# Kernel optimization log

Measured on AMD Instinct MI355X. Metric: run time of the kernel, lower is better.

Reference implementation:

```python
import jax, jax.numpy as jnp
import numpy as np

D_MODEL = 2048
NUM_HEADS = 16
HEAD_DIM = D_MODEL // NUM_HEADS
BATCH = 2
SEQ = 2048


def setup_inputs() -> dict:
    key = jax.random.key(0)
    ks = jax.random.split(key, 5)
    s = 1.0 / np.sqrt(D_MODEL)
    return {
        "x": jax.random.normal(ks[0], (BATCH, SEQ, D_MODEL), dtype=jnp.float32),
        "Wq": jax.random.normal(ks[1], (D_MODEL, D_MODEL), dtype=jnp.float32) * s,
        "Wk": jax.random.normal(ks[2], (D_MODEL, D_MODEL), dtype=jnp.float32) * s,
        "Wv": jax.random.normal(ks[3], (D_MODEL, D_MODEL), dtype=jnp.float32) * s,
        "Wo": jax.random.normal(ks[4], (D_MODEL, D_MODEL), dtype=jnp.float32) * s,
    }


def reference(x, Wq, Wk, Wv, Wo):
    B, S, D = x.shape
    H, Dh = NUM_HEADS, HEAD_DIM
    # nn.Linear(bias=False): y = x @ W.T ; split_heads is a plain view (no transpose!)
    Q = (x @ Wq.T).reshape(B, H, S, Dh)
    K = (x @ Wk.T).reshape(B, H, S, Dh)
    V = (x @ Wv.T).reshape(B, H, S, Dh)
    # scores scaled by head_dim (NOT sqrt) — faithful to source
    scores = jnp.einsum("bhqd,bhkd->bhqk", Q, K) / jnp.float32(Dh)
    causal_mask = jnp.triu(jnp.ones((S, S), dtype=bool), k=1)  # True above diagonal
    scores = jnp.where(causal_mask, -jnp.inf, scores)
    attn = jax.nn.softmax(scores, axis=-1)
    out = jnp.einsum("bhqk,bhkd->bhqd", attn, V)  # [B,H,S,Dh]
    out = out.transpose(0, 2, 1, 3).reshape(B, S, D)  # merge DOES transpose
    return out @ Wo.T
```

## Files before the change

kernel.cpp:

```cpp
#include <hip/hip_runtime.h>
#include <hip/hip_bf16.h>

using bf16 = __hip_bfloat16;
typedef __attribute__((ext_vector_type(8))) short bf16x8;
typedef __attribute__((ext_vector_type(4))) float f32x4;

#define DEVI __device__ __forceinline__

constexpr int Bn = 2, Sn = 2048, Dn = 2048, Hn = 16, DHn = 128;
constexpr int Mn = Bn * Sn;

DEVI void gload_lds16(const bf16* g, bf16* l) {
  __builtin_amdgcn_global_load_lds(
      (__attribute__((address_space(1))) void*)g,
      (__attribute__((address_space(3))) void*)l,
      16, 0, 0);
}

__global__ __launch_bounds__(256) void cvt_all_k(const float* __restrict__ x,
                                                 const float* __restrict__ wq,
                                                 const float* __restrict__ wk,
                                                 const float* __restrict__ wv,
                                                 const float* __restrict__ wo,
                                                 bf16* __restrict__ xb,
                                                 bf16* __restrict__ wb) {
  const int which = blockIdx.y;
  const float* src;
  bf16* dst;
  int n8;
  if (which == 0) { src = x;  dst = xb; n8 = Mn * Dn / 8; }
  else {
    src = (which == 1) ? wq : (which == 2) ? wk : (which == 3) ? wv : wo;
    dst = wb + (size_t)(which - 1) * Dn * Dn;
    n8 = Dn * Dn / 8;
  }
  for (int i = blockIdx.x * 256 + threadIdx.x; i < n8; i += gridDim.x * 256) {
    const float4* p = (const float4*)src + (size_t)i * 2;
    float4 a = p[0], b = p[1];
    union { bf16 h[8]; bf16x8 v; } u;
    u.h[0] = __float2bfloat16(a.x); u.h[1] = __float2bfloat16(a.y);
    u.h[2] = __float2bfloat16(a.z); u.h[3] = __float2bfloat16(a.w);
    u.h[4] = __float2bfloat16(b.x); u.h[5] = __float2bfloat16(b.y);
    u.h[6] = __float2bfloat16(b.z); u.h[7] = __float2bfloat16(b.w);
    *((bf16x8*)dst + i) = u.v;
  }
}

template <int OUTF32, int NCT, int NMAT>
__global__ __launch_bounds__(512, 1) void gemm8f(const bf16* __restrict__ A,
                                                 const bf16* __restrict__ W,
                                                 void* __restrict__ Cv) {
  constexpr int K = 2048, NT = K / 64;
  constexpr int SLOTE = (128 + 256) * 64;
  __shared__ bf16 smem[3 * SLOTE];

  constexpr int MT = Mn / 128;
  const int nwg = MT * NCT;
  const int orig = blockIdx.x;
  const int wgid = (orig & 7) * (nwg >> 3) + (orig >> 3);
  const int bm = wgid / NCT;
  const int bcn = wgid % NCT;
  constexpr int nper = NCT / NMAT;
  const int z = bcn / nper;
  const int col0 = (bcn % nper) * 256;

  const int t = threadIdx.x;
  const int wave = t >> 6, lane = t & 63;
  const int wm = wave >> 2, wn = wave & 3;
  const int lr = lane & 15, lg = lane >> 4;
  const int swz = lr & 7;

  const int srow = t >> 3;
  const int schk = (t & 7) ^ (srow & 7);
  const bf16* Ab = A + (size_t)(bm * 128 + srow) * K + schk * 8;
  const bf16* Bb = W + (size_t)z * (2048 * 2048) +
                   (size_t)(col0 + srow) * K + schk * 8;

  auto stgA = [&](int slot, int kt, int u) {
    gload_lds16(Ab + (size_t)u * 64 * K + kt * 64,
                smem + slot * SLOTE + u * 4096 + t * 8);
  };
  auto stgB = [&](int slot, int kt, int u) {
    gload_lds16(Bb + (size_t)u * 64 * K + kt * 64,
                smem + slot * SLOTE + 8192 + u * 4096 + t * 8);
  };

  f32x4 acc[4][4];
  const f32x4 zf = {0.f, 0.f, 0.f, 0.f};
#pragma unroll
  for (int i = 0; i < 4; ++i)
#pragma unroll
    for (int j = 0; j < 4; ++j) acc[i][j] = zf;

  stgA(0, 0, 0); stgA(0, 0, 1);
  stgB(0, 0, 0); stgB(0, 0, 1); stgB(0, 0, 2); stgB(0, 0, 3);
  stgA(1, 1, 0); stgA(1, 1, 1);
  stgB(1, 1, 0); stgB(1, 1, 1); stgB(1, 1, 2); stgB(1, 1, 3);

  int sl = 0;
#pragma unroll 1
  for (int kt = 0; kt < NT; ++kt) {
    const bf16* sA = smem + sl * SLOTE;
    const bf16* sB = sA + 8192;
    int sl2 = sl + 2; if (sl2 >= 3) sl2 -= 3;
    const bool pf = (kt + 2 < NT);

    if (kt == NT - 1) asm volatile("s_waitcnt vmcnt(0)" ::: "memory");
    else              asm volatile("s_waitcnt vmcnt(6)" ::: "memory");
    __builtin_amdgcn_s_barrier();

    {
      bf16x8 af[4], bv[4];
#pragma unroll
      for (int i = 0; i < 4; ++i)
        af[i] = *(const bf16x8*)(sA + (wm * 64 + i * 16 + lr) * 64 + ((lg ^ swz) * 8));
#pragma unroll
      for (int n = 0; n < 4; ++n)
        bv[n] = *(const bf16x8*)(sB + (wn * 64 + n * 16 + lr) * 64 + ((lg ^ swz) * 8));
      if (pf) { stgA(sl2, kt + 2, 0); stgA(sl2, kt + 2, 1); stgB(sl2, kt + 2, 0); }
      __builtin_amdgcn_s_barrier();
      asm volatile("s_waitcnt lgkmcnt(0)" ::: "memory");
      __builtin_amdgcn_sched_barrier(0);
      __builtin_amdgcn_s_setprio(1);
#pragma unroll
      for (int i = 0; i < 4; ++i)
#pragma unroll
        for (int n = 0; n < 4; ++n)
          acc[i][n] = __builtin_amdgcn_mfma_f32_16x16x32_bf16(af[i], bv[n], acc[i][n], 0, 0, 0);
      __builtin_amdgcn_s_setprio(0);
      __builtin_amdgcn_s_barrier();
    }

    {
      bf16x8 af[4], bv[4];
#pragma unroll
      for (int i = 0; i < 4; ++i)
        af[i] = *(const bf16x8*)(sA + (wm * 64 + i * 16 + lr) * 64 + (((4 + lg) ^ swz) * 8));
#pragma unroll
      for (int n = 0; n < 4; ++n)
        bv[n] = *(const bf16x8*)(sB + (wn * 64 + n * 16 + lr) * 64 + (((4 + lg) ^ swz) * 8));
      if (pf) { stgB(sl2, kt + 2, 1); stgB(sl2, kt + 2, 2); stgB(sl2, kt + 2, 3); }
      __builtin_amdgcn_s_barrier();
      asm volatile("s_waitcnt lgkmcnt(0)" ::: "memory");
      __builtin_amdgcn_sched_barrier(0);
      __builtin_amdgcn_s_setprio(1);
#pragma unroll
      for (int i = 0; i < 4; ++i)
#pragma unroll
        for (int n = 0; n < 4; ++n)
          acc[i][n] = __builtin_amdgcn_mfma_f32_16x16x32_bf16(af[i], bv[n], acc[i][n], 0, 0, 0);
      __builtin_amdgcn_s_setprio(0);
    }

    sl = (sl == 2) ? 0 : sl + 1;
  }

  const int r0 = bm * 128 + wm * 64, c0 = col0 + wn * 64;
#pragma unroll
  for (int mm = 0; mm < 4; ++mm)
#pragma unroll
    for (int nn = 0; nn < 4; ++nn) {
      const int rr = r0 + mm * 16 + lg * 4;
      const int cc = c0 + nn * 16 + lr;
#pragma unroll
      for (int r = 0; r < 4; ++r) {
        float v = acc[mm][nn][r];
        if (OUTF32) {
          ((float*)Cv)[(size_t)(rr + r) * 2048 + cc] = v;
        } else {
          bf16* C = (bf16*)Cv + (size_t)z * (Mn * 2048);
          C[(size_t)(rr + r) * 2048 + cc] = __float2bfloat16(v);
        }
      }
    }
}

__global__ __launch_bounds__(256, 2) void transpose_v(const bf16* __restrict__ V,
                                                      bf16* __restrict__ VT) {
  __shared__ bf16 tile[128 * 128];
  const int kt = blockIdx.x, bh = blockIdx.y;
  const bf16* Vh = V + (size_t)bh * (Sn * DHn);
  bf16* VTh = VT + (size_t)bh * (DHn * Sn);
  const int t = threadIdx.x;
  const int rr = t >> 4, cc = t & 15;
#pragma unroll
  for (int i = 0; i < 8; ++i) {
    int r = rr + i * 16;
    int ch = cc ^ ((r >> 3) & 7);
    *(bf16x8*)(tile + r * 128 + ch * 8) =
        *(const bf16x8*)(Vh + (size_t)(kt * 128 + r) * DHn + cc * 8);
  }
  __syncthreads();
  const int dr = t >> 4, li = t & 15;
#pragma unroll
  for (int i = 0; i < 8; ++i) {
    int dh = dr + i * 16;
    union { bf16 h[8]; bf16x8 v; } u;
#pragma unroll
    for (int j = 0; j < 8; ++j) {
      int k = li * 8 + j;
      int ch = (dh >> 3) ^ ((k >> 3) & 7);
      u.h[j] = tile[k * 128 + ch * 8 + (dh & 7)];
    }
    *(bf16x8*)(VTh + (size_t)dh * Sn + kt * 128 + li * 8) = u.v;
  }
}

__global__ __launch_bounds__(512, 1) void attn_k3(const bf16* __restrict__ Q,
                                                  const bf16* __restrict__ K,
                                                  const bf16* __restrict__ VT,
                                                  bf16* __restrict__ Mg) {
  __shared__ bf16 smem[40960];
  bf16* sK0 = smem;
  bf16* sK1 = smem + 8192;
  bf16* sV0 = smem + 16384;
  bf16* sV1 = smem + 24576;
  bf16* sP  = smem + 32768;
  bf16* sO  = smem;

  const int bi = blockIdx.x;
  const int xcd = bi & 7, slt = bi >> 3;
  const int bh = (slt & 3) * 8 + xcd;
  const int j = slt >> 2;
  const bf16* Qh = Q + (size_t)bh * (Sn * DHn);
  const bf16* Kh = K + (size_t)bh * (Sn * DHn);
  const bf16* VTh = VT + (size_t)bh * (DHn * Sn);
  const int b = bh >> 4, h = bh & 15;

  const int t = threadIdx.x, wave = t >> 6, lane = t & 63;
  const int lr = lane & 15, lg = lane >> 4;

  auto STAGE = [&](int buf, int kt) {
    bf16* dK = buf ? sK1 : sK0;
    bf16* dV = buf ? sV1 : sV0;
#pragma unroll
    for (int i = 0; i < 2; ++i) {
      int c = i * 512 + t;
      int row = c >> 4, c16 = c & 15;
      gload_lds16(Kh + (size_t)(kt * 64 + row) * DHn + ((c16 ^ (row & 7)) * 8),
                  dK + c * 8);
    }
#pragma unroll
    for (int i = 0; i < 2; ++i) {
      int c = i * 512 + t;
      int row = c >> 3, c8 = c & 7;
      gload_lds16(VTh + (size_t)row * Sn + kt * 64 + ((c8 ^ (row & 7)) * 8),
                  dV + c * 8);
    }
  };

  const f32x4 zf = {0.f, 0.f, 0.f, 0.f};

  for (int pi = 0; pi < 2; ++pi) {
    const int qb = pi ? (15 - j) : j;
    const int nt = qb * 2 + 2;
    const int q0 = qb * 128 + wave * 16;

    bf16x8 qf[4];
#pragma unroll
    for (int kk = 0; kk < 4; ++kk)
      qf[kk] = *(const bf16x8*)(Qh + (size_t)(q0 + lr) * DHn + kk * 32 + lg * 8);

    f32x4 o[8];
#pragma unroll
    for (int d = 0; d < 8; ++d) o[d] = zf;
    float mrun[4], lrun[4];
#pragma unroll
    for (int r = 0; r < 4; ++r) { mrun[r] = -3e38f; lrun[r] = 0.f; }

    STAGE(0, 0);
    __syncthreads();
    int cur = 0;

    for (int kt = 0; kt < nt; ++kt) {
      if (kt + 1 < nt) STAGE(cur ^ 1, kt + 1);

      bf16* sKc = cur ? sK1 : sK0;
      bf16* sVc = cur ? sV1 : sV0;

      f32x4 sfr[4];
#pragma unroll
      for (int nn = 0; nn < 4; ++nn) sfr[nn] = zf;
#pragma unroll
      for (int kk = 0; kk < 4; ++kk)
#pragma unroll
        for (int nn = 0; nn < 4; ++nn) {
          int row = nn * 16 + lr;
          int ch = (kk * 4 + lg) ^ (row & 7);
          bf16x8 kf = *(const bf16x8*)(sKc + row * DHn + ch * 8);
          sfr[nn] = __builtin_amdgcn_mfma_f32_16x16x32_bf16(qf[kk], kf, sfr[nn], 0, 0, 0);
        }

      const bool maskt = (kt >= qb * 2);
      float pv[4][4];
#pragma unroll
      for (int nn = 0; nn < 4; ++nn)
#pragma unroll
        for (int r = 0; r < 4; ++r) {
          float v = sfr[nn][r] * (1.0f / 128.0f);
          if (maskt) {
            int kg = kt * 64 + nn * 16 + lr;
            int qg = q0 + lg * 4 + r;
            if (kg > qg) v = -1e30f;
          }
          pv[nn][r] = v;
        }
      float mnew[4], alpha[4], rsum[4];
#pragma unroll
      for (int r = 0; r < 4; ++r) {
        float rm = fmaxf(fmaxf(pv[0][r], pv[1][r]), fmaxf(pv[2][r], pv[3][r]));
        rm = fmaxf(rm, __shfl_xor(rm, 1));
        rm = fmaxf(rm, __shfl_xor(rm, 2));
        rm = fmaxf(rm, __shfl_xor(rm, 4));
        rm = fmaxf(rm, __shfl_xor(rm, 8));
        mnew[r] = fmaxf(mrun[r], rm);
        alpha[r] = __expf(mrun[r] - mnew[r]);
        mrun[r] = mnew[r];
        rsum[r] = 0.f;
      }
#pragma unroll
      for (int nn = 0; nn < 4; ++nn)
#pragma unroll
        for (int r = 0; r < 4; ++r) {
          float p = __expf(pv[nn][r] - mnew[r]);
          pv[nn][r] = p;
          rsum[r] += p;
        }
#pragma unroll
      for (int r = 0; r < 4; ++r) {
        float s = rsum[r];
        s += __shfl_xor(s, 1); s += __shfl_xor(s, 2);
        s += __shfl_xor(s, 4); s += __shfl_xor(s, 8);
        lrun[r] = lrun[r] * alpha[r] + s;
      }
#pragma unroll
      for (int d = 0; d < 8; ++d)
#pragma unroll
        for (int r = 0; r < 4; ++r) o[d][r] *= alpha[r];

#pragma unroll
      for (int nn = 0; nn < 4; ++nn)
#pragma unroll
        for (int r = 0; r < 4; ++r) {
          int row = lg * 4 + r;
          int chk = (nn * 2 + (lr >> 3)) ^ (row & 7);
          sP[wave * 1024 + row * 64 + chk * 8 + (lr & 7)] = __float2bfloat16(pv[nn][r]);
        }

      bf16x8 pf[2];
#pragma unroll
      for (int kk = 0; kk < 2; ++kk) {
        int ch = (kk * 4 + lg) ^ (lr & 7);
        pf[kk] = *(const bf16x8*)(sP + wave * 1024 + lr * 64 + ch * 8);
      }
#pragma unroll
      for (int d = 0; d < 8; ++d)
#pragma unroll
        for (int kk = 0; kk < 2; ++kk) {
          int vrow = d * 16 + lr;
          int vch = (kk * 4 + lg) ^ (vrow & 7);
          bf16x8 vf = *(const bf16x8*)(sVc + vrow * 64 + vch * 8);
          o[d] = __builtin_amdgcn_mfma_f32_16x16x32_bf16(pf[kk], vf, o[d], 0, 0, 0);
        }

      __syncthreads();
      cur ^= 1;
    }

    float inv[4];
#pragma unroll
    for (int r = 0; r < 4; ++r) inv[r] = 1.0f / lrun[r];
#pragma unroll
    for (int d = 0; d < 8; ++d)
#pragma unroll
      for (int r = 0; r < 4; ++r) {
        int row = wave * 16 + lg * 4 + r;
        int col = d * 16 + lr;
        int chk = ((col >> 3) ^ (row & 7));
        sO[row * 128 + chk * 8 + (col & 7)] = __float2bfloat16(o[d][r] * inv[r]);
      }
    __syncthreads();
    bf16* Mh = Mg + ((size_t)(b * Sn + qb * 128)) * Dn + h * DHn;
#pragma unroll
    for (int i = 0; i < 4; ++i) {
      int row = (t >> 4) + i * 32;
      int c16 = t & 15;
      *(bf16x8*)(Mh + (size_t)row * Dn + c16 * 8) =
          *(const bf16x8*)(sO + row * 128 + ((c16 ^ (row & 7)) * 8));
    }
    __syncthreads();
  }
}

extern "C" void kernel_launch(void* const* d_in, const int* in_sizes, int n_in,
                              void* d_out, int out_size, void* d_ws, size_t ws_size,
                              hipStream_t stream) {
  const float* x = (const float*)d_in[0];
  const float* Wq = (const float*)d_in[1];
  const float* Wk = (const float*)d_in[2];
  const float* Wv = (const float*)d_in[3];
  const float* Wo = (const float*)d_in[4];
  float* out = (float*)d_out;

  char* ws = (char*)d_ws;
  bf16* xb = (bf16*)ws;            ws += (size_t)Mn * Dn * 2;
  bf16* Wb = (bf16*)ws;            ws += (size_t)4 * Dn * Dn * 2;
  bf16* QKV = (bf16*)ws;           ws += (size_t)3 * Mn * Dn * 2;
  bf16* VT = (bf16*)ws;            ws += (size_t)Bn * Hn * DHn * Sn * 2;
  bf16* Mg = (bf16*)ws;            ws += (size_t)Mn * Dn * 2;

  cvt_all_k<<<dim3(2048, 5), 256, 0, stream>>>(x, Wq, Wk, Wv, Wo, xb, Wb);

  gemm8f<0, 24, 3><<<768, 512, 0, stream>>>(xb, Wb, (void*)QKV);

  transpose_v<<<dim3(16, 32), 256, 0, stream>>>(QKV + 2 * (size_t)Mn * Dn, VT);

  attn_k3<<<256, 512, 0, stream>>>(QKV, QKV + (size_t)Mn * Dn, VT, Mg);

  gemm8f<1, 8, 1><<<256, 512, 0, stream>>>(Mg, Wb + 3 * (size_t)Dn * Dn, (void*)out);
}
```

Measured before the change: 257.0 us.

## Add 256-thread QKV GEMM kernel and triple-buffer attention K/V staging

After: 251.3 us. 2.2% less time.

```diff
diff --git a/kernel.cpp b/kernel.cpp
--- a/kernel.cpp
+++ b/kernel.cpp
@@ -46,10 +46,119 @@
   }
 }
 
-template <int OUTF32, int NCT, int NMAT>
+template <int NTOT, int NMAT>
+__global__ __launch_bounds__(256, 2) void gemmY(const bf16* __restrict__ A,
+                                                const bf16* __restrict__ W,
+                                                bf16* __restrict__ Cv) {
+  constexpr int K = 2048, NT = 64;
+  __shared__ bf16 smem[2 * 12288];
+
+  const int nwg = NTOT * 16;
+  const int orig = blockIdx.x;
+  const int wgid = (orig & 7) * (nwg >> 3) + (orig >> 3);
+  const int bm = wgid / NTOT;
+  const int bnn = wgid % NTOT;
+  constexpr int nper = NTOT / NMAT;
+  const int z = bnn / nper;
+  const int col0 = (bnn % nper) * 128;
+
+  const int t = threadIdx.x;
+  const int wave = t >> 6, lane = t & 63;
+  const int wm = wave >> 1, wn = wave & 1;
+  const int lr = lane & 15, lg = lane >> 4;
+  const int rch = ((lg ^ ((lr >> 1) & 3)) * 8);
+  const int srow = t >> 2;
+  const int sch = (t & 3) ^ ((t >> 3) & 3);
+
+  const bf16* Ab = A + (size_t)(bm * 256 + srow) * K + sch * 8;
+  const bf16* Bb = W + (size_t)z * (2048 * 2048) +
+                   (size_t)(col0 + srow) * K + sch * 8;
+
+  auto stgA = [&](int slot, int kt, int u) {
+    gload_lds16(Ab + (size_t)u * 64 * K + kt * 32,
+                smem + slot * 12288 + u * 2048 + t * 8);
+  };
+  auto stgB = [&](int slot, int kt, int v) {
+    gload_lds16(Bb + (size_t)v * 64 * K + kt * 32,
+                smem + slot * 12288 + 8192 + v * 2048 + t * 8);
+  };
+
+  f32x4 acc[8][4];
+  const f32x4 zf = {0.f, 0.f, 0.f, 0.f};
+#pragma unroll
+  for (int i = 0; i < 8; ++i)
+#pragma unroll
+    for (int j = 0; j < 4; ++j) acc[i][j] = zf;
+
+  stgA(0, 0, 0); stgA(0, 0, 1); stgA(0, 0, 2); stgA(0, 0, 3);
+  stgB(0, 0, 0); stgB(0, 0, 1);
+  stgA(1, 1, 0); stgA(1, 1, 2); stgB(1, 1, 0); stgB(1, 1, 1);
+
+#pragma unroll 2
+  for (int kt = 0; kt < NT; ++kt) {
+    const int slot = kt & 1;
+    const bf16* sAb = smem + slot * 12288;
+    const bf16* sBb = sAb + 8192;
+
+    if (kt == NT - 1) asm volatile("s_waitcnt vmcnt(0)" ::: "memory");
+    else              asm volatile("s_waitcnt vmcnt(4)" ::: "memory");
+    __builtin_amdgcn_s_barrier();
+
+    bf16x8 af[4], bv[4];
+#pragma unroll
+    for (int i = 0; i < 4; ++i)
+      af[i] = *(const bf16x8*)(sAb + (wm * 128 + i * 16 + lr) * 32 + rch);
+#pragma unroll
+    for (int n = 0; n < 4; ++n)
+      bv[n] = *(const bf16x8*)(sBb + (wn * 64 + n * 16 + lr) * 32 + rch);
+    if (kt + 1 < NT) { stgA(slot ^ 1, kt + 1, 1); stgA(slot ^ 1, kt + 1, 3); }
+    asm volatile("s_waitcnt lgkmcnt(0)" ::: "memory");
+    __builtin_amdgcn_sched_barrier(0);
+    __builtin_amdgcn_s_setprio(1);
+#pragma unroll
+    for (int i = 0; i < 4; ++i)
+#pragma unroll
+      for (int n = 0; n < 4; ++n)
+        acc[i][n] = __builtin_amdgcn_mfma_f32_16x16x32_bf16(af[i], bv[n], acc[i][n], 0, 0, 0);
+    __builtin_amdgcn_s_setprio(0);
+    __builtin_amdgcn_s_barrier();
+
+#pragma unroll
+    for (int i = 0; i < 4; ++i)
+      af[i] = *(const bf16x8*)(sAb + (wm * 128 + 64 + i * 16 + lr) * 32 + rch);
+    if (kt + 2 < NT) {
+      stgA(slot, kt + 2, 0); stgA(slot, kt + 2, 2);
+      stgB(slot, kt + 2, 0); stgB(slot, kt + 2, 1);
+    }
+    asm volatile("s_waitcnt lgkmcnt(0)" ::: "memory");
+    __builtin_amdgcn_sched_barrier(0);
+    __builtin_amdgcn_s_setprio(1);
+#pragma unroll
+    for (int i = 0; i < 4; ++i)
+#pragma unroll
+      for (int n = 0; n < 4; ++n)
+        acc[4 + i][n] = __builtin_amdgcn_mfma_f32_16x16x32_bf16(af[i], bv[n], acc[4 + i][n], 0, 0, 0);
+    __builtin_amdgcn_s_setprio(0);
+  }
+
+  const int r0 = bm * 256 + wm * 128, c0 = col0 + wn * 64;
+#pragma unroll
+  for (int mm = 0; mm < 8; ++mm)
+#pragma unroll
+    for (int nn = 0; nn < 4; ++nn) {
+      const int rr = r0 + mm * 16 + lg * 4;
+      const int cc = c0 + nn * 16 + lr;
+      bf16* C = Cv + (size_t)z * (Mn * 2048);
+#pragma unroll
+      for (int r = 0; r < 4; ++r)
+        C[(size_t)(rr + r) * 2048 + cc] = __float2bfloat16(acc[mm][nn][r]);
+    }
+}
+
+template <int NCT>
 __global__ __launch_bounds__(512, 1) void gemm8f(const bf16* __restrict__ A,
                                                  const bf16* __restrict__ W,
-                                                 void* __restrict__ Cv) {
+                                                 float* __restrict__ Cv) {
   constexpr int K = 2048, NT = K / 64;
   constexpr int SLOTE = (128 + 256) * 64;
   __shared__ bf16 smem[3 * SLOTE];
@@ -60,9 +169,7 @@
   const int wgid = (orig & 7) * (nwg >> 3) + (orig >> 3);
   const int bm = wgid / NCT;
   const int bcn = wgid % NCT;
-  constexpr int nper = NCT / NMAT;
-  const int z = bcn / nper;
-  const int col0 = (bcn % nper) * 256;
+  const int col0 = bcn * 256;
 
   const int t = threadIdx.x;
   const int wave = t >> 6, lane = t & 63;
@@ -73,8 +180,7 @@
   const int srow = t >> 3;
   const int schk = (t & 7) ^ (srow & 7);
   const bf16* Ab = A + (size_t)(bm * 128 + srow) * K + schk * 8;
-  const bf16* Bb = W + (size_t)z * (2048 * 2048) +
-                   (size_t)(col0 + srow) * K + schk * 8;
+  const bf16* Bb = W + (size_t)(col0 + srow) * K + schk * 8;
 
   auto stgA = [&](int slot, int kt, int u) {
     gload_lds16(Ab + (size_t)u * 64 * K + kt * 64,
@@ -130,7 +236,6 @@
       __builtin_amdgcn_s_setprio(0);
       __builtin_amdgcn_s_barrier();
     }
-
     {
       bf16x8 af[4], bv[4];
 #pragma unroll
@@ -151,7 +256,6 @@
           acc[i][n] = __builtin_amdgcn_mfma_f32_16x16x32_bf16(af[i], bv[n], acc[i][n], 0, 0, 0);
       __builtin_amdgcn_s_setprio(0);
     }
-
     sl = (sl == 2) ? 0 : sl + 1;
   }
 
@@ -163,15 +267,8 @@
       const int rr = r0 + mm * 16 + lg * 4;
       const int cc = c0 + nn * 16 + lr;
 #pragma unroll
-      for (int r = 0; r < 4; ++r) {
-        float v = acc[mm][nn][r];
-        if (OUTF32) {
-          ((float*)Cv)[(size_t)(rr + r) * 2048 + cc] = v;
-        } else {
-          bf16* C = (bf16*)Cv + (size_t)z * (Mn * 2048);
-          C[(size_t)(rr + r) * 2048 + cc] = __float2bfloat16(v);
-        }
-      }
+      for (int r = 0; r < 4; ++r)
+        Cv[(size_t)(rr + r) * 2048 + cc] = acc[mm][nn][r];
     }
 }
 
@@ -206,17 +303,13 @@
   }
 }
 
-__global__ __launch_bounds__(512, 1) void attn_k3(const bf16* __restrict__ Q,
+__global__ __launch_bounds__(512, 1) void attn_k4(const bf16* __restrict__ Q,
                                                   const bf16* __restrict__ K,
                                                   const bf16* __restrict__ VT,
                                                   bf16* __restrict__ Mg) {
-  __shared__ bf16 smem[40960];
-  bf16* sK0 = smem;
-  bf16* sK1 = smem + 8192;
-  bf16* sV0 = smem + 16384;
-  bf16* sV1 = smem + 24576;
-  bf16* sP  = smem + 32768;
-  bf16* sO  = smem;
+  __shared__ bf16 smem[57344];
+  bf16* sP = smem + 49152;
+  bf16* sO = smem;
 
   const int bi = blockIdx.x;
   const int xcd = bi & 7, slt = bi >> 3;
@@ -230,9 +323,9 @@
   const int t = threadIdx.x, wave = t >> 6, lane = t & 63;
   const int lr = lane & 15, lg = lane >> 4;
 
-  auto STAGE = [&](int buf, int kt) {
-    bf16* dK = buf ? sK1 : sK0;
-    bf16* dV = buf ? sV1 : sV0;
+  auto STAGE = [&](int s, int kt) {
+    bf16* dK = smem + s * 16384;
+    bf16* dV = dK + 8192;
 #pragma unroll
     for (int i = 0; i < 2; ++i) {
       int c = i * 512 + t;
@@ -269,14 +362,16 @@
     for (int r = 0; r < 4; ++r) { mrun[r] = -3e38f; lrun[r] = 0.f; }
 
     STAGE(0, 0);
-    __syncthreads();
-    int cur = 0;
+    STAGE(1, 1);
+    asm volatile("s_waitcnt vmcnt(4)" ::: "memory");
+    __builtin_amdgcn_s_barrier();
 
     for (int kt = 0; kt < nt; ++kt) {
-      if (kt + 1 < nt) STAGE(cur ^ 1, kt + 1);
-
-      bf16* sKc = cur ? sK1 : sK0;
-      bf16* sVc = cur ? sV1 : sV0;
+      const int sl = kt % 3;
+      if (kt + 2 < nt) STAGE((kt + 2) % 3, kt + 2);
+
+      bf16* sKc = smem + sl * 16384;
+      bf16* sVc = sKc + 8192;
 
       f32x4 sfr[4];
 #pragma unroll
@@ -363,8 +458,9 @@
           o[d] = __builtin_amdgcn_mfma_f32_16x16x32_bf16(pf[kk], vf, o[d], 0, 0, 0);
         }
 
-      __syncthreads();
-      cur ^= 1;
+      if (kt + 2 < nt) asm volatile("s_waitcnt vmcnt(4)" ::: "memory");
+      else             asm volatile("s_waitcnt vmcnt(0)" ::: "memory");
+      __builtin_amdgcn_s_barrier();
     }
 
     float inv[4];
@@ -411,11 +507,11 @@
 
   cvt_all_k<<<dim3(2048, 5), 256, 0, stream>>>(x, Wq, Wk, Wv, Wo, xb, Wb);
 
-  gemm8f<0, 24, 3><<<768, 512, 0, stream>>>(xb, Wb, (void*)QKV);
+  gemmY<48, 3><<<768, 256, 0, stream>>>(xb, Wb, QKV);
 
   transpose_v<<<dim3(16, 32), 256, 0, stream>>>(QKV + 2 * (size_t)Mn * Dn, VT);
 
-  attn_k3<<<256, 512, 0, stream>>>(QKV, QKV + (size_t)Mn * Dn, VT, Mg);
-
-  gemm8f<1, 8, 1><<<256, 512, 0, stream>>>(Mg, Wb + 3 * (size_t)Dn * Dn, (void*)out);
-}
+  attn_k4<<<256, 512, 0, stream>>>(QKV, QKV + (size_t)Mn * Dn, VT, Mg);
+
+  gemm8f<8><<<256, 512, 0, stream>>>(Mg, Wb + 3 * (size_t)Dn * Dn, out);
+}
```
